# Kernel optimization log

Measured on AMD Instinct MI355X. Metric: run time of the kernel, lower is better.

## Reference

```python
import jax, jax.numpy as jnp
import numpy as np

N, T, D, H = 4, 2048, 512, 8
HD = D // H  # head dim = split size


def setup_inputs() -> dict:
    key = jax.random.key(0)
    k1, k2, k3, k4 = jax.random.split(key, 4)
    scale = 1.0 / np.sqrt(D)
    return {
        "query": jax.random.normal(k1, (N, T, D), dtype=jnp.float32),
        "Wk": jax.random.normal(k2, (D, D), dtype=jnp.float32) * scale,
        "Wv": jax.random.normal(k3, (D, D), dtype=jnp.float32) * scale,
        "Wo": jax.random.normal(k4, (D, D), dtype=jnp.float32) * scale,
    }


def reference(query, Wk, Wv, Wo):
    # torch.nn.Linear(x) == x @ W.T (no bias)
    querys = query                              # [N, T, D]
    keys = query @ Wk.T + query                 # residual-added keys [N, T, D]
    values = query @ Wv.T                       # [N, T, D]

    # split along feature dim into H heads, stacked on a leading head axis
    def split_heads(x):
        # [N, T, D] -> [H, N, T, HD]
        return jnp.transpose(x.reshape(N, T, H, HD), (2, 0, 1, 3))

    q = split_heads(querys)
    k = split_heads(keys)
    v = split_heads(values)

    scores = jnp.einsum("hnqd,hnkd->hnqk", q, k) / np.sqrt(HD).astype(np.float32)
    scores = jax.nn.softmax(scores, axis=3)      # [H, N, Tq, Tk]
    out = jnp.einsum("hnqk,hnkd->hnqd", scores, v)

    # concat heads back along feature dim: [H, N, T, HD] -> [N, T, D]
    out = jnp.transpose(out, (1, 2, 0, 3)).reshape(N, T, D)
    out = out @ Wo.T
    return out
```

## Files before the change

### kernel.cpp

```cpp
#include <hip/hip_runtime.h>
#include <cstdint>
#include <cstddef>

#define NB 4
#define TS 2048
#define DM 512
#define HN 8
#define HD 64

typedef __attribute__((ext_vector_type(8))) short bf16x8;
typedef __attribute__((ext_vector_type(16))) float f32x16;
typedef __attribute__((ext_vector_type(4))) float f32x4;
typedef __attribute__((ext_vector_type(4))) short short4v;
typedef __attribute__((ext_vector_type(4))) unsigned u32x4;

static __device__ __forceinline__ short f2bf(float f) {
  unsigned u = __float_as_uint(f);
  unsigned r = (u + 0x7fffu + ((u >> 16) & 1u)) >> 16;
  return (short)r;
}

static __device__ __forceinline__ float bf2f(short s) {
  return __uint_as_float(((unsigned)(unsigned short)s) << 16);
}

static __device__ __forceinline__ unsigned cvtpk(float lo, float hi) {
  unsigned r;
  asm("v_cvt_pk_bf16_f32 %0, %1, %2" : "=v"(r) : "v"(lo), "v"(hi));
  return r;
}

static __device__ __forceinline__ void plane32swap(unsigned& x, unsigned& y) {
  asm volatile("v_permlane32_swap_b32 %0, %1" : "+v"(x), "+v"(y));
}

static __device__ __forceinline__ void gload16(const void* g, void* l) {
  __builtin_amdgcn_global_load_lds(
      (const __attribute__((address_space(1))) void*)g,
      (__attribute__((address_space(3))) void*)l, 16, 0, 0);
}

#define WAIT_VM(N) asm volatile("s_waitcnt vmcnt(" #N ")" ::: "memory")
#define BAR() __builtin_amdgcn_s_barrier()

#define MFMA16(a, b, c) __builtin_amdgcn_mfma_f32_16x16x32_bf16((a), (b), (c), 0, 0, 0)
#define MFMA32(a, b, c) __builtin_amdgcn_mfma_f32_32x32x16_bf16((a), (b), (c), 0, 0, 0)

__global__ __launch_bounds__(256) void cast_all(const float* __restrict__ Q,
                                                const float* __restrict__ Wk,
                                                const float* __restrict__ Wv,
                                                const float* __restrict__ Wo,
                                                short* __restrict__ Qb,
                                                short* __restrict__ Wb) {
  int i = blockIdx.x * 256 + threadIdx.x;
  const int Q4 = (NB * TS * DM) / 4;
  const float* src;
  short* dst;
  int off;
  if (i < Q4) {
    src = Q; dst = Qb; off = i;
  } else {
    int j = i - Q4;
    int which = j >> 16;
    off = j & 65535;
    src = which == 0 ? Wk : (which == 1 ? Wv : Wo);
    dst = Wb + ((size_t)which << 18);
  }
  float4 v = reinterpret_cast<const float4*>(src)[off];
  short4v o;
  o.x = f2bf(v.x);
  o.y = f2bf(v.y);
  o.z = f2bf(v.z);
  o.w = f2bf(v.w);
  reinterpret_cast<short4v*>(dst)[off] = o;
}

__global__ __launch_bounds__(256) void gemm_kv(const short* __restrict__ Qb,
                                               const short* __restrict__ Wkb,
                                               const short* __restrict__ Wvb,
                                               const float* __restrict__ resid,
                                               short* __restrict__ Kb,
                                               short* __restrict__ Vt) {
  __shared__ alignas(16) short lA[2][128 * 32];
  __shared__ alignas(16) short lK[2][64 * 32];
  __shared__ alignas(16) short lV[2][64 * 32];
  const int row0 = blockIdx.x * 128;
  const int col0 = blockIdx.y * 64;
  const int tid = threadIdx.x;
  const int lane = tid & 63;
  const int wave = tid >> 6;
  const int wr = wave >> 1, wc = wave & 1;
  const int fr = lane & 15, fk = (lane >> 4) * 8;

  f32x4 kacc[4][2], vacc[2][4];
  const f32x4 z4 = {0.f, 0.f, 0.f, 0.f};
#pragma unroll
  for (int m = 0; m < 4; ++m)
#pragma unroll
    for (int nn = 0; nn < 2; ++nn) {
      kacc[m][nn] = z4;
      vacc[nn][m] = z4;
    }

  const int sr = tid >> 2;
  const int sc8 = (tid & 3) * 8;

#define GSTAGE(buf, kt)                                                 \
  do {                                                                  \
    gload16(&Qb[(size_t)(row0 + sr) * DM + (kt) + sc8],                 \
            (char*)&lA[(buf)][0] + (size_t)tid * 16);                   \
    gload16(&Qb[(size_t)(row0 + 64 + sr) * DM + (kt) + sc8],            \
            (char*)&lA[(buf)][0] + 4096 + (size_t)tid * 16);            \
    gload16(&Wkb[(size_t)(col0 + sr) * DM + (kt) + sc8],                \
            (char*)&lK[(buf)][0] + (size_t)tid * 16);                   \
    gload16(&Wvb[(size_t)(col0 + sr) * DM + (kt) + sc8],                \
            (char*)&lV[(buf)][0] + (size_t)tid * 16);                   \
  } while (0)

  GSTAGE(0, 0);
  __syncthreads();
  int cur = 0;
  for (int kt = 0; kt < 16; ++kt) {
    if (kt < 15) GSTAGE(cur ^ 1, (kt + 1) * 32);
    bf16x8 af[4], bk[2], bv[2];
#pragma unroll
    for (int m = 0; m < 4; ++m)
      af[m] = *reinterpret_cast<const bf16x8*>(&lA[cur][(wr * 64 + m * 16 + fr) * 32 + fk]);
#pragma unroll
    for (int nn = 0; nn < 2; ++nn) {
      bk[nn] = *reinterpret_cast<const bf16x8*>(&lK[cur][(wc * 32 + nn * 16 + fr) * 32 + fk]);
      bv[nn] = *reinterpret_cast<const bf16x8*>(&lV[cur][(wc * 32 + nn * 16 + fr) * 32 + fk]);
    }
    __builtin_amdgcn_s_setprio(1);
#pragma unroll
    for (int m = 0; m < 4; ++m)
#pragma unroll
      for (int nn = 0; nn < 2; ++nn) {
        kacc[m][nn] = MFMA16(af[m], bk[nn], kacc[m][nn]);
        vacc[nn][m] = MFMA16(bv[nn], af[m], vacc[nn][m]);
      }
    __builtin_amdgcn_s_setprio(0);
    __syncthreads();
    cur ^= 1;
  }
#undef GSTAGE

#pragma unroll
  for (int m = 0; m < 4; ++m) {
#pragma unroll
    for (int nn = 0; nn < 2; ++nn) {
#pragma unroll
      for (int i = 0; i < 4; ++i) {
        int gr = row0 + wr * 64 + m * 16 + (lane >> 4) * 4 + i;
        int gc = col0 + wc * 32 + nn * 16 + fr;
        float v = kacc[m][nn][i] + resid[(size_t)gr * DM + gc];
        Kb[(size_t)gr * DM + gc] = f2bf(v);
      }
    }
  }
#pragma unroll
  for (int nn = 0; nn < 2; ++nn) {
#pragma unroll
    for (int m = 0; m < 4; ++m) {
#pragma unroll
      for (int i = 0; i < 4; ++i) {
        int d = col0 + wc * 32 + nn * 16 + (lane >> 4) * 4 + i;
        int q = row0 + wr * 64 + m * 16 + fr;
        int nb = q >> 11, t = q & (TS - 1);
        Vt[((size_t)nb * DM + d) * TS + t] = f2bf(vacc[nn][m][i]);
      }
    }
  }
}

__global__ __launch_bounds__(256) void gemm_o(const short* __restrict__ A,
                                              const short* __restrict__ W,
                                              float* __restrict__ out0) {
  __shared__ alignas(16) short lA[2][128 * 32];
  __shared__ alignas(16) short lB[2][64 * 32];
  const int row0 = blockIdx.x * 128;
  const int col0 = blockIdx.y * 64;
  const int tid = threadIdx.x;
  const int lane = tid & 63;
  const int wave = tid >> 6;
  const int wr = wave >> 1, wc = wave & 1;
  const int fr = lane & 15, fk = (lane >> 4) * 8;

  f32x4 acc[4][2];
  const f32x4 z4 = {0.f, 0.f, 0.f, 0.f};
#pragma unroll
  for (int m = 0; m < 4; ++m)
#pragma unroll
    for (int nn = 0; nn < 2; ++nn) acc[m][nn] = z4;

  const int sr = tid >> 2;
  const int sc8 = (tid & 3) * 8;

#define GSTAGE(buf, kt)                                                \
  do {                                                                 \
    gload16(&A[(size_t)(row0 + sr) * DM + (kt) + sc8],                 \
            (char*)&lA[(buf)][0] + (size_t)tid * 16);                  \
    gload16(&A[(size_t)(row0 + 64 + sr) * DM + (kt) + sc8],            \
            (char*)&lA[(buf)][0] + 4096 + (size_t)tid * 16);           \
    gload16(&W[(size_t)(col0 + sr) * DM + (kt) + sc8],                 \
            (char*)&lB[(buf)][0] + (size_t)tid * 16);                  \
  } while (0)

  GSTAGE(0, 0);
  __syncthreads();
  int cur = 0;
  for (int kt = 0; kt < 16; ++kt) {
    if (kt < 15) GSTAGE(cur ^ 1, (kt + 1) * 32);
    bf16x8 af[4], bfr[2];
#pragma unroll
    for (int m = 0; m < 4; ++m)
      af[m] = *reinterpret_cast<const bf16x8*>(&lA[cur][(wr * 64 + m * 16 + fr) * 32 + fk]);
#pragma unroll
    for (int nn = 0; nn < 2; ++nn)
      bfr[nn] = *reinterpret_cast<const bf16x8*>(&lB[cur][(wc * 32 + nn * 16 + fr) * 32 + fk]);
    __builtin_amdgcn_s_setprio(1);
#pragma unroll
    for (int m = 0; m < 4; ++m)
#pragma unroll
      for (int nn = 0; nn < 2; ++nn) acc[m][nn] = MFMA16(af[m], bfr[nn], acc[m][nn]);
    __builtin_amdgcn_s_setprio(0);
    __syncthreads();
    cur ^= 1;
  }
#undef GSTAGE

#pragma unroll
  for (int m = 0; m < 4; ++m)
#pragma unroll
    for (int nn = 0; nn < 2; ++nn)
#pragma unroll
      for (int i = 0; i < 4; ++i) {
        int gr = row0 + wr * 64 + m * 16 + (lane >> 4) * 4 + i;
        int gc = col0 + wc * 32 + nn * 16 + fr;
        out0[(size_t)gr * DM + gc] = acc[m][nn][i];
      }
}

__global__ __launch_bounds__(512, 4) void attn(const short* __restrict__ Qb,
                                               const short* __restrict__ Kb,
                                               const short* __restrict__ Vt,
                                               short* __restrict__ Ob) {
  __shared__ alignas(16) short kv[2][2][2][64 * 64];
  const int bid = blockIdx.x;
  const int blk = (bid & 7) * 64 + (bid >> 3);
  const int qt = blk & 15;
  const int nh = blk >> 4;
  const int h = nh & (HN - 1);
  const int n = nh >> 3;
  const int wv = threadIdx.x >> 6, lane = threadIdx.x & 63;
  const int grp = wv >> 2, qs = wv & 3;
  const int l31 = lane & 31, hf = lane >> 5;
  const int q0 = qt * 128 + qs * 32;
  const float SC2 = 0.18033688011f;

  bf16x8 qf[4];
  const short* qrow = Qb + (size_t)(n * TS + q0 + l31) * DM + h * HD;
#pragma unroll
  for (int ks = 0; ks < 4; ++ks) {
    bf16x8 t = *reinterpret_cast<const bf16x8*>(qrow + ks * 16 + hf * 8);
#pragma unroll
    for (int j = 0; j < 8; ++j) t[j] = f2bf(bf2f(t[j]) * SC2);
    qf[ks] = t;
  }

  bf16x8 ones;
#pragma unroll
  for (int i = 0; i < 8; ++i) ones[i] = (short)0x3F80;

  f32x16 o0, o1, osum;
#pragma unroll
  for (int r = 0; r < 16; ++r) {
    o0[r] = 0.f;
    o1[r] = 0.f;
    osum[r] = 0.f;
  }

  const int srow8 = lane >> 3;
  const int scol = ((lane & 7) ^ srow8) * 8;
  const int swz = (l31 & 7) << 4;
  const int tbase = grp * 16;

#define STAGE(buf, t)                                                                 \
  do {                                                                                \
    int r0_ = qs * 16 + srow8;                                                        \
    int r1_ = r0_ + 8;                                                                \
    char* kb_ = (char*)&kv[grp][(buf)][0][0] + qs * 2048;                             \
    char* vb_ = (char*)&kv[grp][(buf)][1][0] + qs * 2048;                             \
    gload16(Kb + (size_t)(n * TS + (t) * 64 + r0_) * DM + h * HD + scol, kb_);        \
    gload16(Kb + (size_t)(n * TS + (t) * 64 + r1_) * DM + h * HD + scol, kb_ + 1024); \
    gload16(Vt + ((size_t)(nh * HD + r0_) * TS + (t) * 64 + scol), vb_);              \
    gload16(Vt + ((size_t)(nh * HD + r1_) * TS + (t) * 64 + scol), vb_ + 1024);       \
  } while (0)

  STAGE(0, tbase);

  int cur = 0;
  for (int j = 0; j < 16; ++j) {
    if (j < 15) {
      STAGE(cur ^ 1, tbase + j + 1);
      WAIT_VM(4);
    } else {
      WAIT_VM(0);
    }
    BAR();

    const char* Kl = (const char*)&kv[grp][cur][0][0];
    const char* Vl = (const char*)&kv[grp][cur][1][0];

    f32x16 s0, s1;
#pragma unroll
    for (int r = 0; r < 16; ++r) {
      s0[r] = 0.f;
      s1[r] = 0.f;
    }
    __builtin_amdgcn_s_setprio(1);
#pragma unroll
    for (int ks = 0; ks < 4; ++ks) {
      int colb = ks * 32 + hf * 16;
      bf16x8 ka0 = *reinterpret_cast<const bf16x8*>(Kl + l31 * 128 + (colb ^ swz));
      bf16x8 ka1 = *reinterpret_cast<const bf16x8*>(Kl + (l31 + 32) * 128 + (colb ^ swz));
      s0 = MFMA32(ka0, qf[ks], s0);
      s1 = MFMA32(ka1, qf[ks], s1);
    }
    __builtin_amdgcn_s_setprio(0);

#pragma unroll
    for (int r = 0; r < 16; ++r) {
      s0[r] = __builtin_amdgcn_exp2f(s0[r]);
      s1[r] = __builtin_amdgcn_exp2f(s1[r]);
    }

    unsigned w0[4][2], w1[4][2];
#pragma unroll
    for (int c = 0; c < 4; ++c) {
      w0[c][0] = cvtpk(s0[4 * c], s0[4 * c + 1]);
      w0[c][1] = cvtpk(s0[4 * c + 2], s0[4 * c + 3]);
      w1[c][0] = cvtpk(s1[4 * c], s1[4 * c + 1]);
      w1[c][1] = cvtpk(s1[4 * c + 2], s1[4 * c + 3]);
    }

    __builtin_amdgcn_s_setprio(1);
#pragma unroll
    for (int ks = 0; ks < 4; ++ks) {
      const int ce = (ks & 1) * 2, co = ce + 1;
      unsigned xa = (ks < 2) ? w0[ce][0] : w1[ce][0];
      unsigned xb = (ks < 2) ? w0[ce][1] : w1[ce][1];
      unsigned ya = (ks < 2) ? w0[co][0] : w1[co][0];
      unsigned yb = (ks < 2) ? w0[co][1] : w1[co][1];
      plane32swap(xa, ya);
      plane32swap(xb, yb);
      u32x4 pw;
      pw.x = xa;
      pw.y = xb;
      pw.z = ya;
      pw.w = yb;
      bf16x8 pa = *reinterpret_cast<bf16x8*>(&pw);

      int colb = ks * 32 + hf * 16;
      bf16x8 v0 = *reinterpret_cast<const bf16x8*>(Vl + l31 * 128 + (colb ^ swz));
      bf16x8 v1 = *reinterpret_cast<const bf16x8*>(Vl + (l31 + 32) * 128 + (colb ^ swz));
      o0 = MFMA32(pa, v0, o0);
      o1 = MFMA32(pa, v1, o1);
      osum = MFMA32(pa, ones, osum);
    }
    __builtin_amdgcn_s_setprio(0);

    BAR();
    cur ^= 1;
  }
#undef STAGE

  float* sp = (float*)&kv[0][0][0][0];
  const int sbase = (qs * 64 + lane) * 49;
  if (grp == 1) {
#pragma unroll
    for (int r = 0; r < 16; ++r) {
      sp[sbase + r] = o0[r];
      sp[sbase + 16 + r] = o1[r];
      sp[sbase + 32 + r] = osum[r];
    }
  }
  __syncthreads();
  if (grp == 0) {
#pragma unroll
    for (int r = 0; r < 16; ++r) {
      o0[r] += sp[sbase + r];
      o1[r] += sp[sbase + 16 + r];
      osum[r] += sp[sbase + 32 + r];
    }
#pragma unroll
    for (int r = 0; r < 16; ++r) {
      int q = q0 + (r & 3) + 8 * (r >> 2) + 4 * hf;
      float is = 1.0f / osum[r];
      size_t base = (size_t)(n * TS + q) * DM + h * HD;
      Ob[base + l31] = f2bf(o0[r] * is);
      Ob[base + 32 + l31] = f2bf(o1[r] * is);
    }
  }
}

extern "C" void kernel_launch(void* const* d_in, const int* in_sizes, int n_in,
                              void* d_out, int out_size, void* d_ws, size_t ws_size,
                              hipStream_t stream) {
  (void)in_sizes; (void)n_in; (void)out_size; (void)ws_size;
  const float* Q = (const float*)d_in[0];
  const float* Wk = (const float*)d_in[1];
  const float* Wv = (const float*)d_in[2];
  const float* Wo = (const float*)d_in[3];

  const size_t QE = (size_t)NB * TS * DM;
  const size_t WE = (size_t)DM * DM;
  short* ws = (short*)d_ws;
  short* Qb = ws;
  short* Kb = Qb + QE;
  short* Vt = Kb + QE;
  short* Ao = Vt + QE;
  short* Wkb = Ao + QE;
  short* Wvb = Wkb + WE;
  short* Wob = Wvb + WE;

  {
    int total4 = (int)((QE + 3 * WE) / 4);
    cast_all<<<total4 / 256, 256, 0, stream>>>(Q, Wk, Wv, Wo, Qb, Wkb);
  }
  {
    dim3 g(64, 8);
    gemm_kv<<<g, 256, 0, stream>>>(Qb, Wkb, Wvb, Q, Kb, Vt);
  }
  attn<<<NB * HN * (TS / 128), 512, 0, stream>>>(Qb, Kb, Vt, Ao);
  {
    dim3 g(64, 8);
    gemm_o<<<g, 256, 0, stream>>>(Ao, Wob, (float*)d_out);
  }
}
```

Before: 86.36 us.

## Fold residual into Wk and write K/V in MFMA-fragment-packed layout

The identity is added to Wk during the bf16 cast, so the K projection computes Q(Wk+I)^T and no longer reads the fp32 residual in the gemm epilogue. gemm_kv now writes K and V directly in a per-head, per-tile layout that matches the attention MFMA operand fragments, using 8-byte vector stores instead of scalar 2-byte stores. The attention kernel then stages contiguous 4 KB chunks and reads LDS with linear per-lane offsets, with no swizzle or strided global gathers. Rounding Wk+I to bf16 loses a little precision on the diagonal compared with adding the residual in fp32.

Measured after the change: 79.71 us. 1.08x faster.

```diff
diff --git a/kernel.cpp b/kernel.cpp
--- a/kernel.cpp
+++ b/kernel.cpp
@@ -57,16 +57,29 @@
   const float* src;
   short* dst;
   int off;
+  int which = -1;
   if (i < Q4) {
     src = Q; dst = Qb; off = i;
   } else {
     int j = i - Q4;
-    int which = j >> 16;
+    which = j >> 16;
     off = j & 65535;
     src = which == 0 ? Wk : (which == 1 ? Wv : Wo);
     dst = Wb + ((size_t)which << 18);
   }
   float4 v = reinterpret_cast<const float4*>(src)[off];
+  if (which == 0) {
+    int e0 = off * 4;
+    int row = e0 >> 9;
+    int col0 = e0 & 511;
+    if (row >= col0 && row < col0 + 4) {
+      int c = row - col0;
+      if (c == 0) v.x += 1.0f;
+      else if (c == 1) v.y += 1.0f;
+      else if (c == 2) v.z += 1.0f;
+      else v.w += 1.0f;
+    }
+  }
   short4v o;
   o.x = f2bf(v.x);
   o.y = f2bf(v.y);
@@ -78,28 +91,28 @@
 __global__ __launch_bounds__(256) void gemm_kv(const short* __restrict__ Qb,
                                                const short* __restrict__ Wkb,
                                                const short* __restrict__ Wvb,
-                                               const float* __restrict__ resid,
-                                               short* __restrict__ Kb,
-                                               short* __restrict__ Vt) {
+                                               short* __restrict__ KP,
+                                               short* __restrict__ VP) {
   __shared__ alignas(16) short lA[2][128 * 32];
   __shared__ alignas(16) short lK[2][64 * 32];
   __shared__ alignas(16) short lV[2][64 * 32];
   const int row0 = blockIdx.x * 128;
-  const int col0 = blockIdx.y * 64;
+  const int col0d = blockIdx.y * 64;
   const int tid = threadIdx.x;
   const int lane = tid & 63;
   const int wave = tid >> 6;
   const int wr = wave >> 1, wc = wave & 1;
   const int fr = lane & 15, fk = (lane >> 4) * 8;
-
-  f32x4 kacc[4][2], vacc[2][4];
+  const int g = lane >> 4;
+
+  f32x4 kacc[2][4], vacc[4][2];
   const f32x4 z4 = {0.f, 0.f, 0.f, 0.f};
 #pragma unroll
   for (int m = 0; m < 4; ++m)
 #pragma unroll
     for (int nn = 0; nn < 2; ++nn) {
-      kacc[m][nn] = z4;
-      vacc[nn][m] = z4;
+      kacc[nn][m] = z4;
+      vacc[m][nn] = z4;
     }
 
   const int sr = tid >> 2;
@@ -111,9 +124,9 @@
             (char*)&lA[(buf)][0] + (size_t)tid * 16);                   \
     gload16(&Qb[(size_t)(row0 + 64 + sr) * DM + (kt) + sc8],            \
             (char*)&lA[(buf)][0] + 4096 + (size_t)tid * 16);            \
-    gload16(&Wkb[(size_t)(col0 + sr) * DM + (kt) + sc8],                \
+    gload16(&Wkb[(size_t)(col0d + sr) * DM + (kt) + sc8],               \
             (char*)&lK[(buf)][0] + (size_t)tid * 16);                   \
-    gload16(&Wvb[(size_t)(col0 + sr) * DM + (kt) + sc8],                \
+    gload16(&Wvb[(size_t)(col0d + sr) * DM + (kt) + sc8],               \
             (char*)&lV[(buf)][0] + (size_t)tid * 16);                   \
   } while (0)
 
@@ -122,22 +135,22 @@
   int cur = 0;
   for (int kt = 0; kt < 16; ++kt) {
     if (kt < 15) GSTAGE(cur ^ 1, (kt + 1) * 32);
-    bf16x8 af[4], bk[2], bv[2];
+    bf16x8 af[4], wk[2], wv[2];
 #pragma unroll
     for (int m = 0; m < 4; ++m)
       af[m] = *reinterpret_cast<const bf16x8*>(&lA[cur][(wr * 64 + m * 16 + fr) * 32 + fk]);
 #pragma unroll
     for (int nn = 0; nn < 2; ++nn) {
-      bk[nn] = *reinterpret_cast<const bf16x8*>(&lK[cur][(wc * 32 + nn * 16 + fr) * 32 + fk]);
-      bv[nn] = *reinterpret_cast<const bf16x8*>(&lV[cur][(wc * 32 + nn * 16 + fr) * 32 + fk]);
+      wk[nn] = *reinterpret_cast<const bf16x8*>(&lK[cur][(wc * 32 + nn * 16 + fr) * 32 + fk]);
+      wv[nn] = *reinterpret_cast<const bf16x8*>(&lV[cur][(wc * 32 + nn * 16 + fr) * 32 + fk]);
     }
     __builtin_amdgcn_s_setprio(1);
 #pragma unroll
     for (int m = 0; m < 4; ++m)
 #pragma unroll
       for (int nn = 0; nn < 2; ++nn) {
-        kacc[m][nn] = MFMA16(af[m], bk[nn], kacc[m][nn]);
-        vacc[nn][m] = MFMA16(bv[nn], af[m], vacc[nn][m]);
+        kacc[nn][m] = MFMA16(wk[nn], af[m], kacc[nn][m]);
+        vacc[m][nn] = MFMA16(af[m], wv[nn], vacc[m][nn]);
       }
     __builtin_amdgcn_s_setprio(0);
     __syncthreads();
@@ -146,29 +159,39 @@
 #undef GSTAGE
 
 #pragma unroll
+  for (int nn = 0; nn < 2; ++nn) {
+#pragma unroll
+    for (int m = 0; m < 4; ++m) {
+      int d = col0d + wc * 32 + nn * 16 + g * 4;
+      int kseq = row0 + wr * 64 + m * 16 + fr;
+      int h = d >> 6, dd = d & 63;
+      int n = kseq >> 11, kk = kseq & (TS - 1);
+      int t = kk >> 6, H = (kk >> 5) & 1;
+      int ks = (dd >> 4) & 3, hfd = (dd >> 3) & 1, jb = dd & 7;
+      int slot = (kk & 31) + 32 * hfd;
+      short4v pk;
+#pragma unroll
+      for (int i = 0; i < 4; ++i) pk[i] = f2bf(kacc[nn][m][i]);
+      size_t addr = ((((size_t)(n * HN + h) * 32 + t) * 8 + H * 4 + ks) * 64 + slot) * 8 + jb;
+      *reinterpret_cast<short4v*>(&KP[addr]) = pk;
+    }
+  }
+#pragma unroll
   for (int m = 0; m < 4; ++m) {
 #pragma unroll
     for (int nn = 0; nn < 2; ++nn) {
-#pragma unroll
-      for (int i = 0; i < 4; ++i) {
-        int gr = row0 + wr * 64 + m * 16 + (lane >> 4) * 4 + i;
-        int gc = col0 + wc * 32 + nn * 16 + fr;
-        float v = kacc[m][nn][i] + resid[(size_t)gr * DM + gc];
-        Kb[(size_t)gr * DM + gc] = f2bf(v);
-      }
-    }
-  }
-#pragma unroll
-  for (int nn = 0; nn < 2; ++nn) {
-#pragma unroll
-    for (int m = 0; m < 4; ++m) {
-#pragma unroll
-      for (int i = 0; i < 4; ++i) {
-        int d = col0 + wc * 32 + nn * 16 + (lane >> 4) * 4 + i;
-        int q = row0 + wr * 64 + m * 16 + fr;
-        int nb = q >> 11, t = q & (TS - 1);
-        Vt[((size_t)nb * DM + d) * TS + t] = f2bf(vacc[nn][m][i]);
-      }
+      int kseq = row0 + wr * 64 + m * 16 + g * 4;
+      int d = col0d + wc * 32 + nn * 16 + fr;
+      int h = d >> 6, dd = d & 63;
+      int n = kseq >> 11, kk = kseq & (TS - 1);
+      int t = kk >> 6, hfk = (kk >> 3) & 1, jb = kk & 7;
+      int ksV = (kk >> 4) & 3, D = (dd >> 5) & 1;
+      int slot = (dd & 31) + 32 * hfk;
+      short4v pv;
+#pragma unroll
+      for (int i = 0; i < 4; ++i) pv[i] = f2bf(vacc[m][nn][i]);
+      size_t addr = ((((size_t)(n * HN + h) * 32 + t) * 8 + D * 4 + ksV) * 64 + slot) * 8 + jb;
+      *reinterpret_cast<short4v*>(&VP[addr]) = pv;
     }
   }
 }
@@ -242,8 +265,8 @@
 }
 
 __global__ __launch_bounds__(512, 4) void attn(const short* __restrict__ Qb,
-                                               const short* __restrict__ Kb,
-                                               const short* __restrict__ Vt,
+                                               const short* __restrict__ KP,
+                                               const short* __restrict__ VP,
                                                short* __restrict__ Ob) {
   __shared__ alignas(16) short kv[2][2][2][64 * 64];
   const int bid = blockIdx.x;
@@ -280,25 +303,24 @@
     osum[r] = 0.f;
   }
 
-  const int srow8 = lane >> 3;
-  const int scol = ((lane & 7) ^ srow8) * 8;
-  const int swz = (l31 & 7) << 4;
   const int tbase = grp * 16;
-
-#define STAGE(buf, t)                                                                 \
-  do {                                                                                \
-    int r0_ = qs * 16 + srow8;                                                        \
-    int r1_ = r0_ + 8;                                                                \
-    char* kb_ = (char*)&kv[grp][(buf)][0][0] + qs * 2048;                             \
-    char* vb_ = (char*)&kv[grp][(buf)][1][0] + qs * 2048;                             \
-    gload16(Kb + (size_t)(n * TS + (t) * 64 + r0_) * DM + h * HD + scol, kb_);        \
-    gload16(Kb + (size_t)(n * TS + (t) * 64 + r1_) * DM + h * HD + scol, kb_ + 1024); \
-    gload16(Vt + ((size_t)(nh * HD + r0_) * TS + (t) * 64 + scol), vb_);              \
-    gload16(Vt + ((size_t)(nh * HD + r1_) * TS + (t) * 64 + scol), vb_ + 1024);       \
+  const size_t nhbase = (size_t)nh * 32 * 4096;
+
+#define STAGE(buf, t)                                                           \
+  do {                                                                          \
+    const short* kS = KP + nhbase + (size_t)(t) * 4096 + qs * 1024 + lane * 8;  \
+    const short* vS = VP + nhbase + (size_t)(t) * 4096 + qs * 1024 + lane * 8;  \
+    char* kb_ = (char*)&kv[grp][(buf)][0][0] + qs * 2048;                       \
+    char* vb_ = (char*)&kv[grp][(buf)][1][0] + qs * 2048;                       \
+    gload16(kS, kb_);                                                           \
+    gload16(kS + 512, kb_ + 1024);                                              \
+    gload16(vS, vb_);                                                           \
+    gload16(vS + 512, vb_ + 1024);                                              \
   } while (0)
 
   STAGE(0, tbase);
 
+  const int lb = lane * 16;
   int cur = 0;
   for (int j = 0; j < 16; ++j) {
     if (j < 15) {
@@ -321,9 +343,8 @@
     __builtin_amdgcn_s_setprio(1);
 #pragma unroll
     for (int ks = 0; ks < 4; ++ks) {
-      int colb = ks * 32 + hf * 16;
-      bf16x8 ka0 = *reinterpret_cast<const bf16x8*>(Kl + l31 * 128 + (colb ^ swz));
-      bf16x8 ka1 = *reinterpret_cast<const bf16x8*>(Kl + (l31 + 32) * 128 + (colb ^ swz));
+      bf16x8 ka0 = *reinterpret_cast<const bf16x8*>(Kl + ks * 1024 + lb);
+      bf16x8 ka1 = *reinterpret_cast<const bf16x8*>(Kl + (4 + ks) * 1024 + lb);
       s0 = MFMA32(ka0, qf[ks], s0);
       s1 = MFMA32(ka1, qf[ks], s1);
     }
@@ -361,9 +382,8 @@
       pw.w = yb;
       bf16x8 pa = *reinterpret_cast<bf16x8*>(&pw);
 
-      int colb = ks * 32 + hf * 16;
-      bf16x8 v0 = *reinterpret_cast<const bf16x8*>(Vl + l31 * 128 + (colb ^ swz));
-      bf16x8 v1 = *reinterpret_cast<const bf16x8*>(Vl + (l31 + 32) * 128 + (colb ^ swz));
+      bf16x8 v0 = *reinterpret_cast<const bf16x8*>(Vl + ks * 1024 + lb);
+      bf16x8 v1 = *reinterpret_cast<const bf16x8*>(Vl + (4 + ks) * 1024 + lb);
       o0 = MFMA32(pa, v0, o0);
       o1 = MFMA32(pa, v1, o1);
       osum = MFMA32(pa, ones, osum);
@@ -417,9 +437,9 @@
   const size_t WE = (size_t)DM * DM;
   short* ws = (short*)d_ws;
   short* Qb = ws;
-  short* Kb = Qb + QE;
-  short* Vt = Kb + QE;
-  short* Ao = Vt + QE;
+  short* KP = Qb + QE;
+  short* VP = KP + QE;
+  short* Ao = VP + QE;
   short* Wkb = Ao + QE;
   short* Wvb = Wkb + WE;
   short* Wob = Wvb + WE;
@@ -430,9 +450,9 @@
   }
   {
     dim3 g(64, 8);
-    gemm_kv<<<g, 256, 0, stream>>>(Qb, Wkb, Wvb, Q, Kb, Vt);
-  }
-  attn<<<NB * HN * (TS / 128), 512, 0, stream>>>(Qb, Kb, Vt, Ao);
+    gemm_kv<<<g, 256, 0, stream>>>(Qb, Wkb, Wvb, KP, VP);
+  }
+  attn<<<NB * HN * (TS / 128), 512, 0, stream>>>(Qb, KP, VP, Ao);
   {
     dim3 g(64, 8);
     gemm_o<<<g, 256, 0, stream>>>(Ao, Wob, (float*)d_out);
```
